# Performance work log

Hardware: AMD Instinct MI355X
Metric: run time of the kernel (lower is better)

## Reference

```python
import jax, jax.numpy as jnp
import numpy as np
from jax import lax


def _gru(x, h, Wi, Wh, bi, bh):
    # PyTorch GRUCell: gates ordered (r, z, n)
    gi = x @ Wi + bi
    gh = h @ Wh + bh
    ir, iz, in_ = jnp.split(gi, 3, axis=-1)
    hr, hz, hn = jnp.split(gh, 3, axis=-1)
    r = jax.nn.sigmoid(ir + hr)
    z = jax.nn.sigmoid(iz + hz)
    n = jnp.tanh(in_ + r * hn)
    return (1.0 - z) * n + z * h


def _mlp(x, W1, b1, W2, b2):
    return jax.nn.leaky_relu(x @ W1 + b1, 0.1) @ W2 + b2


def setup_inputs() -> dict:
    key = jax.random.key(0)
    S, Wn, E, DH, OD = 128, 3968, 128, 512, 2  # scenarios, world agents, embed, dec hidden, out dim
    N, H = S + Wn, 4 * E
    ks = jax.random.split(key, 32)
    rn = lambda k, sh, s: (jax.random.normal(k, sh, jnp.float32) * s)
    # ragged segment ids: every scenario gets >=1 world agent, rest random
    extra = jax.random.randint(ks[0], (Wn - S,), 0, S)
    seg_ids = jnp.sort(jnp.concatenate([jnp.arange(S), extra])).astype(jnp.int32)
    sH = 1.0 / np.sqrt(H)
    return {
        'goals': rn(ks[1], (N, 2), 1.0),
        'agn_dyn': rn(ks[2], (N, E), 1.0),
        'agn_ccls': rn(ks[3], (N, E), 1.0),
        'agn_int': rn(ks[4], (N, E), 1.0),
        'seg_ids': seg_ids,
        'sdc_h0': rn(ks[5], (S, H), 1.0),
        'wld_h0': rn(ks[6], (Wn, H), 1.0),
        'gol_W': rn(ks[7], (2, E), 1.0 / np.sqrt(2.0)),
        'gol_b': rn(ks[8], (E,), 0.01),
        'sdc_Wi': rn(ks[9], (H, 3 * H), sH), 'sdc_Wh': rn(ks[10], (H, 3 * H), sH),
        'sdc_bi': rn(ks[11], (3 * H,), 0.01), 'sdc_bh': rn(ks[12], (3 * H,), 0.01),
        'wld_Wi': rn(ks[13], (H, 3 * H), sH), 'wld_Wh': rn(ks[14], (H, 3 * H), sH),
        'wld_bi': rn(ks[15], (3 * H,), 0.01), 'wld_bh': rn(ks[16], (3 * H,), 0.01),
        'sdc_o1W': rn(ks[17], (H, DH), sH), 'sdc_o1b': rn(ks[18], (DH,), 0.01),
        'sdc_o2W': rn(ks[19], (DH, OD), 1.0 / np.sqrt(DH)), 'sdc_o2b': rn(ks[20], (OD,), 0.01),
        'wld_o1W': rn(ks[21], (H, DH), sH), 'wld_o1b': rn(ks[22], (DH,), 0.01),
        'wld_o2W': rn(ks[23], (DH, OD), 1.0 / np.sqrt(DH)), 'wld_o2b': rn(ks[24], (OD,), 0.01),
    }


def reference(goals, agn_dyn, agn_ccls, agn_int, seg_ids, sdc_h0, wld_h0,
              gol_W, gol_b, sdc_Wi, sdc_Wh, sdc_bi, sdc_bh,
              wld_Wi, wld_Wh, wld_bi, wld_bh,
              sdc_o1W, sdc_o1b, sdc_o2W, sdc_o2b,
              wld_o1W, wld_o1b, wld_o2W, wld_o2b):
    S = sdc_h0.shape[0]
    agn_gol = goals @ gol_W + gol_b                                  # [N, E]
    enc = jnp.concatenate([agn_gol, agn_dyn, agn_ccls, agn_int], 1)  # [N, 4E]
    sdc_h = _gru(enc[:S], sdc_h0, sdc_Wi, sdc_Wh, sdc_bi, sdc_bh)    # step 0
    wld_h = _gru(enc[S:], wld_h0, wld_Wi, wld_Wh, wld_bi, wld_bh)

    def step(carry, _):
        sh, wh = carry
        sdc_in = jax.ops.segment_max(wh, seg_ids, num_segments=S,
                                     indices_are_sorted=True)        # per-scenario max-pool
        wld_in = sh[seg_ids]                                         # broadcast SDC to its group
        sh2 = _gru(sdc_in, sh, sdc_Wi, sdc_Wh, sdc_bi, sdc_bh)
        wh2 = _gru(wld_in, wh, wld_Wi, wld_Wh, wld_bi, wld_bh)
        return (sh2, wh2), (sh2, wh2)

    (_, _), (sdc_hs, wld_hs) = lax.scan(step, (sdc_h, wld_h), None, length=79)
    sdc_all = jnp.concatenate([sdc_h[None], sdc_hs], 0).transpose(1, 0, 2)  # [S, 80, 4E]
    wld_all = jnp.concatenate([wld_h[None], wld_hs], 0).transpose(1, 0, 2)  # [W, 80, 4E]
    out_sdc = _mlp(sdc_all, sdc_o1W, sdc_o1b, sdc_o2W, sdc_o2b)
    out_wld = _mlp(wld_all, wld_o1W, wld_o1b, wld_o2W, wld_o2b)
    return jnp.concatenate([out_sdc, out_wld], 0)                    # [N, 80, out_dim]
```

## Files before the change

kernel.cpp:

```cpp
#include <hip/hip_runtime.h>


typedef __attribute__((ext_vector_type(8))) short short8;
typedef __attribute__((ext_vector_type(4))) float f32x4;
typedef unsigned short u16;
typedef unsigned int u32;

#define DEV __device__ __forceinline__

constexpr int S  = 128;
constexpr int NR = 4096;
constexpr int H  = 512;
constexpr int TH = 1536;
constexpr int SLOT = NR * H;
constexpr int SEGSZ = S * H;

struct P {
  const float *goals, *dyn, *ccls, *inte;
  const int *seg;
  const float *sdc_h0, *wld_h0;
  const float *golW, *golb;
  const float *sdcbi, *sdcbh, *wldbi, *wldbh;
  const float *sdco1b, *sdco2W, *sdco2b;
  const float *wldo1b, *wldo2W, *wldo2b;
  const float *sdcWi, *sdcWh, *wldWi, *wldWh, *sdco1W, *wldo1W;
  float *out;
  float *whf;
  u16   *ring;
  u16   *enc;
  u16   *WT;
  u16   *o1T;
  float *G;
  u32   *segb;
  u16   *segbf;
  float *part;
  int t;
};

DEV u16 f2bf(float f) {
  u32 u = __float_as_uint(f);
  u32 r = u + 0x7FFFu + ((u >> 16) & 1u);
  return (u16)(r >> 16);
}
DEV u32 flipf(float f) {
  u32 u = __float_as_uint(f);
  return (u & 0x80000000u) ? ~u : (u | 0x80000000u);
}
DEV float unflip(u32 s) {
  u32 u = (s & 0x80000000u) ? (s & 0x7FFFFFFFu) : ~s;
  return __uint_as_float(u);
}
DEV float sigm(float x)  { return 1.0f / (1.0f + __expf(-x)); }
DEV float tanh_(float x) { return 2.0f / (1.0f + __expf(-2.0f * x)) - 1.0f; }

DEV f32x4 mfma16(short8 a, short8 b, f32x4 c) {
  return __builtin_amdgcn_mfma_f32_16x16x32_bf16(a, b, c, 0, 0, 0);
}

DEV void gload16(const void* g, void* l) {
  __builtin_amdgcn_global_load_lds(
      (const __attribute__((address_space(1))) void*)g,
      (__attribute__((address_space(3))) void*)l, 16, 0, 0);
}

DEV short8 lds_frag(const u16* lds, int row, int g) {
  return *(const short8*)(lds + row * 64 + ((g ^ (row & 7)) << 3));
}

__global__ __launch_bounds__(256) void k_prep(P p) {
  const int b = blockIdx.x, tid = threadIdx.x;
  __shared__ float ltf[64 * 65];
  if (b < 896) {
    int nt, kt, Nn; const float* src; u16* dst;
    if (b < 768) {
      int m = b / 192, t2 = b % 192;
      nt = t2 % 24; kt = t2 / 24; Nn = TH;
      src = (m == 0) ? p.sdcWi : (m == 1) ? p.sdcWh : (m == 2) ? p.wldWi : p.wldWh;
      dst = p.WT + m * TH * H;
    } else {
      int bb = b - 768, m = bb / 64, t2 = bb % 64;
      nt = t2 % 8; kt = t2 / 8; Nn = H;
      src = m ? p.wldo1W : p.sdco1W;
      dst = p.o1T + m * H * H;
    }
    for (int it = 0; it < 16; ++it) {
      int kl = it * 4 + (tid >> 6), nl = tid & 63;
      ltf[nl * 65 + kl] = src[(kt * 64 + kl) * Nn + nt * 64 + nl];
    }
    __syncthreads();
    for (int it = 0; it < 2; ++it) {
      int nl = it * 32 + (tid >> 3), k8 = (tid & 7) * 8;
      short8 v;
#pragma unroll
      for (int e = 0; e < 8; ++e) v[e] = (short)f2bf(ltf[nl * 65 + k8 + e]);
      *(short8*)(dst + (nt * 64 + nl) * H + kt * 64 + k8) = v;
    }
  } else if (b < 960) {
    int r0 = (b - 896) * 64;
    for (int i = 0; i < 32; ++i) {
      int idx = i * 256 + tid;
      int row = r0 + (idx >> 7), c4 = (idx & 127) * 4;
      float4 v;
      if (c4 < 128) {
        float g0 = p.goals[row * 2], g1 = p.goals[row * 2 + 1];
        v.x = g0 * p.golW[c4]     + g1 * p.golW[128 + c4]     + p.golb[c4];
        v.y = g0 * p.golW[c4 + 1] + g1 * p.golW[128 + c4 + 1] + p.golb[c4 + 1];
        v.z = g0 * p.golW[c4 + 2] + g1 * p.golW[128 + c4 + 2] + p.golb[c4 + 2];
        v.w = g0 * p.golW[c4 + 3] + g1 * p.golW[128 + c4 + 3] + p.golb[c4 + 3];
      } else if (c4 < 256) v = *(const float4*)(p.dyn  + row * 128 + c4 - 128);
      else if (c4 < 384)   v = *(const float4*)(p.ccls + row * 128 + c4 - 256);
      else                 v = *(const float4*)(p.inte + row * 128 + c4 - 384);
      ushort4 o;
      o.x = f2bf(v.x); o.y = f2bf(v.y); o.z = f2bf(v.z); o.w = f2bf(v.w);
      *(ushort4*)(p.enc + row * H + c4) = o;
    }
  } else if (b < 1024) {
    int r0 = (b - 960) * 64;
    for (int i = 0; i < 32; ++i) {
      int idx = i * 256 + tid;
      int row = r0 + (idx >> 7), c4 = (idx & 127) * 4;
      float4 v = (row < S) ? *(const float4*)(p.sdc_h0 + row * H + c4)
                           : *(const float4*)(p.wld_h0 + (row - S) * H + c4);
      *(float4*)(p.whf + SLOT + row * H + c4) = v;
      ushort4 o;
      o.x = f2bf(v.x); o.y = f2bf(v.y); o.z = f2bf(v.z); o.w = f2bf(v.w);
      *(ushort4*)(p.ring + 7 * SLOT + row * H + c4) = o;
    }
  } else {
    int base = (b - 1024) * 16384;
    for (int i = 0; i < 64; ++i) p.segb[base + i * 256 + tid] = 0u;
  }
}

__global__ __launch_bounds__(512) void k_big0(P p) {
  const int b = blockIdx.x, tid = threadIdx.x;
  const int rt = b >> 3, cg = b & 7;
  const bool sdc = rt < 2;
  const int wv = tid >> 6, wm = wv >> 2, wn = wv & 3;
  const int lr = (tid >> 4) & 3, lc = tid & 15;
  __shared__ u16 sm[16384];
  const u16* WiT = p.WT + (sdc ? 0 : 2) * TH * H;
  const u16* WhT = p.WT + (sdc ? 1 : 3) * TH * H;

  f32x4 ai[3][2], ah[3][2];
  f32x4 zero = {0.f, 0.f, 0.f, 0.f};
#pragma unroll
  for (int g = 0; g < 3; ++g)
#pragma unroll
    for (int mt = 0; mt < 2; ++mt) { ai[g][mt] = zero; ah[g][mt] = zero; }

  for (int pass = 0; pass < 2; ++pass) {
    const u16* A  = pass ? (p.ring + 7 * SLOT + rt * 64 * H) : (p.enc + rt * 64 * H);
    const u16* BT = pass ? WhT : WiT;
    for (int kc = 0; kc < H; kc += 64) {
      __syncthreads();
#pragma unroll
      for (int it = 0; it < 4; ++it) {
        int u = it * 512 + tid;
        int gs = (u ^ (u >> 3)) & 7;
        const u16* src;
        if (u < 512) {
          src = A + (u >> 3) * H + kc + gs * 8;
        } else {
          int v = u - 512;
          int g = v >> 9, m = (v >> 3) & 63;
          src = BT + (g * H + cg * 64 + m) * H + kc + gs * 8;
        }
        gload16(src, sm + (it * 512 + (tid & 448)) * 8);
      }
      __syncthreads();
#pragma unroll
      for (int s2 = 0; s2 < 2; ++s2) {
        const int gk = s2 * 4 + lr;
        short8 av[2], bv[3];
#pragma unroll
        for (int mt = 0; mt < 2; ++mt)
          av[mt] = lds_frag(sm, wm * 32 + mt * 16 + lc, gk);
#pragma unroll
        for (int g = 0; g < 3; ++g)
          bv[g] = lds_frag(sm + 4096 + g * 4096, wn * 16 + lc, gk);
#pragma unroll
        for (int g = 0; g < 3; ++g)
#pragma unroll
          for (int mt = 0; mt < 2; ++mt) {
            f32x4 r = pass ? ah[g][mt] : ai[g][mt];
            r = mfma16(av[mt], bv[g], r);
            if (pass) ah[g][mt] = r; else ai[g][mt] = r;
          }
      }
    }
  }
  const float* bi = sdc ? p.sdcbi : p.wldbi;
  const float* bh = sdc ? p.sdcbh : p.wldbh;
  const int col = cg * 64 + wn * 16 + lc;
  const float bir = bi[col], biz = bi[H + col], bin = bi[2 * H + col];
  const float bhr = bh[col], bhz = bh[H + col], bhn = bh[2 * H + col];
#pragma unroll
  for (int mt = 0; mt < 2; ++mt)
#pragma unroll
    for (int i = 0; i < 4; ++i) {
      int grow = rt * 64 + wm * 32 + mt * 16 + lr * 4 + i;
      float r = sigm(ai[0][mt][i] + bir + ah[0][mt][i] + bhr);
      float z = sigm(ai[1][mt][i] + biz + ah[1][mt][i] + bhz);
      float n = tanh_(ai[2][mt][i] + bin + r * (ah[2][mt][i] + bhn));
      float h = p.whf[SLOT + grow * H + col];
      float h2 = (1.f - z) * n + z * h;
      p.whf[grow * H + col] = h2;
      p.ring[grow * H + col] = f2bf(h2);
      if (!sdc) {
        int scen = p.seg[grow - S];
        atomicMax(p.segb + scen * H + col, flipf(h2));
      }
    }
}

__global__ __launch_bounds__(512) void k_small(P p) {
  const int b = blockIdx.x, tid = threadIdx.x;
  if (b >= 48) {
    if ((p.t & 7) != 0 || p.t < 8) return;
    const int base = p.t - 8;
    const int gt2 = (b - 48) * 512 + tid;
    for (int i = gt2; i < 65536; i += 32768) {
      int r = i >> 1, od = i & 1;
      int row = r & 4095, slot = r >> 12;
      float v = p.part[i] + p.part[65536 + i];
      v += (row < S ? p.sdco2b : p.wldo2b)[od];
      p.out[row * 160 + (base + slot) * 2 + od] = v;
    }
    return;
  }
  const int gtid = b * 512 + tid;
  u32* sb = p.segb + (p.t & 1) * SEGSZ;
  if (gtid < 16384) ((uint4*)sb)[gtid] = make_uint4(0u, 0u, 0u, 0u);
  const u32* sp = p.segb + ((p.t - 1) & 1) * SEGSZ;
  if (gtid < 16384) {
    uint4 q = ((const uint4*)sp)[gtid];
    u32 lo = (u32)f2bf(unflip(q.x)) | ((u32)f2bf(unflip(q.y)) << 16);
    u32 hi = (u32)f2bf(unflip(q.z)) | ((u32)f2bf(unflip(q.w)) << 16);
    ((u32*)p.segbf)[gtid * 2]     = lo;
    ((u32*)p.segbf)[gtid * 2 + 1] = hi;
  }
  const int rh = b / 24, nc = b % 24;
  const int wv = tid >> 6, wm = wv >> 2, wn = wv & 3;
  const int lr = (tid >> 4) & 3, lc = tid & 15;
  __shared__ u16 sm[16384];
  const u16* Ab = p.ring + ((p.t - 1) & 7) * SLOT + rh * 64 * H;
  const u16* Wb = p.WT + 2 * TH * H;

  f32x4 acc[2];
  f32x4 zero = {0.f, 0.f, 0.f, 0.f};
  acc[0] = zero; acc[1] = zero;

  for (int kc = 0; kc < H; kc += 128) {
    __syncthreads();
#pragma unroll
    for (int it = 0; it < 4; ++it) {
      int u = it * 512 + tid;
      int q = u >> 9;
      int m = (u >> 3) & 63, g = u & 7;
      int gs = g ^ (m & 7);
      int ko = kc + ((q & 1) << 6) + gs * 8;
      const u16* src = (q < 2) ? (Ab + m * H + ko)
                               : (Wb + (nc * 64 + m) * H + ko);
      gload16(src, sm + (it * 512 + (tid & 448)) * 8);
    }
    __syncthreads();
#pragma unroll
    for (int c = 0; c < 2; ++c)
#pragma unroll
      for (int s2 = 0; s2 < 2; ++s2) {
        const int gk = s2 * 4 + lr;
        short8 bv = lds_frag(sm + (2 + c) * 4096, wn * 16 + lc, gk);
#pragma unroll
        for (int mt = 0; mt < 2; ++mt)
          acc[mt] = mfma16(
              lds_frag(sm + c * 4096, wm * 32 + mt * 16 + lc, gk), bv, acc[mt]);
      }
  }
  const int colb = nc * 64 + wn * 16 + lc;
  const float bi = p.wldbi[colb];
#pragma unroll
  for (int mt = 0; mt < 2; ++mt)
#pragma unroll
    for (int i = 0; i < 4; ++i)
      p.G[(rh * 64 + wm * 32 + mt * 16 + lr * 4 + i) * TH + colb] = acc[mt][i] + bi;
}

__global__ __launch_bounds__(512) void k_big(P p) {
  const int b = blockIdx.x, tid = threadIdx.x;
  const int lr = (tid >> 4) & 3, lc = tid & 15;
  __shared__ u16 sm[16384];
  const int tp = (p.t - 1) & 7, tn = p.t & 7;
  const float* whfP = p.whf + ((p.t - 1) & 1) * SLOT;
  float* whfN = p.whf + (p.t & 1) * SLOT;
  u16* ringN = p.ring + tn * SLOT;

  if (b < 496) {
    const int wv = tid >> 6, wm = wv >> 2, wn = wv & 3;
    const int rt = b >> 3, cg = b & 7;
    const u16* Abase = p.ring + tp * SLOT + (S + rt * 64) * H;
    const u16* Bbase = p.WT + 3 * TH * H;
    f32x4 acc[3][2];
    f32x4 zero = {0.f, 0.f, 0.f, 0.f};
#pragma unroll
    for (int g = 0; g < 3; ++g) { acc[g][0] = zero; acc[g][1] = zero; }

    for (int kc = 0; kc < H; kc += 64) {
      __syncthreads();
#pragma unroll
      for (int it = 0; it < 4; ++it) {
        int u = it * 512 + tid;
        int gs = (u ^ (u >> 3)) & 7;
        const u16* src;
        if (u < 512) {
          src = Abase + (u >> 3) * H + kc + gs * 8;
        } else {
          int v = u - 512;
          int g = v >> 9, m = (v >> 3) & 63;
          src = Bbase + (g * H + cg * 64 + m) * H + kc + gs * 8;
        }
        gload16(src, sm + (it * 512 + (tid & 448)) * 8);
      }
      __syncthreads();
#pragma unroll
      for (int s2 = 0; s2 < 2; ++s2) {
        const int gk = s2 * 4 + lr;
        short8 av[2], bv[3];
#pragma unroll
        for (int mt = 0; mt < 2; ++mt)
          av[mt] = lds_frag(sm, wm * 32 + mt * 16 + lc, gk);
#pragma unroll
        for (int g = 0; g < 3; ++g)
          bv[g] = lds_frag(sm + 4096 + g * 4096, wn * 16 + lc, gk);
#pragma unroll
        for (int g = 0; g < 3; ++g)
#pragma unroll
          for (int mt = 0; mt < 2; ++mt) acc[g][mt] = mfma16(av[mt], bv[g], acc[g][mt]);
      }
    }
    const int col = cg * 64 + wn * 16 + lc;
    const float bhr = p.wldbh[col], bhz = p.wldbh[H + col], bhn = p.wldbh[2 * H + col];
    u32* sb = p.segb + (p.t & 1) * SEGSZ;
    int curSc = -1; float curMx = 0.f;
#pragma unroll
    for (int mt = 0; mt < 2; ++mt)
#pragma unroll
      for (int i = 0; i < 4; ++i) {
        int wrow = rt * 64 + wm * 32 + mt * 16 + lr * 4 + i;
        int grow = S + wrow;
        int scen = p.seg[wrow];
        const float* Gr = p.G + scen * TH;
        float r = sigm(Gr[col]          + acc[0][mt][i] + bhr);
        float z = sigm(Gr[H + col]      + acc[1][mt][i] + bhz);
        float n = tanh_(Gr[2 * H + col] + r * (acc[2][mt][i] + bhn));
        float h = whfP[grow * H + col];
        float h2 = (1.f - z) * n + z * h;
        whfN[grow * H + col] = h2;
        ringN[grow * H + col] = f2bf(h2);
        if (scen == curSc) curMx = fmaxf(curMx, h2);
        else {
          if (curSc >= 0) atomicMax(sb + curSc * H + col, flipf(curMx));
          curSc = scen; curMx = h2;
        }
      }
    atomicMax(sb + curSc * H + col, flipf(curMx));
  } else {
    const int w = tid >> 6;
    if (w >= 4) return;
    const int ab = b - 496, rh = ab >> 5, cgx = ab & 31;
    f32x4 ai[3], ah[3];
    f32x4 zero = {0.f, 0.f, 0.f, 0.f};
#pragma unroll
    for (int g = 0; g < 3; ++g) { ai[g] = zero; ah[g] = zero; }

    for (int pass = 0; pass < 2; ++pass) {
      const u16* A  = pass ? (p.ring + tp * SLOT + rh * 64 * H)
                           : (p.segbf + rh * 64 * H);
      const u16* BT = p.WT + (pass ? 1 : 0) * TH * H;
      for (int kc = 0; kc < H; kc += 64) {
        __syncthreads();
#pragma unroll
        for (int it = 0; it < 4; ++it) {
          int u = it * 256 + tid;
          if (u < 896) {
            int gs = (u ^ (u >> 3)) & 7;
            const u16* src;
            if (u < 512) {
              src = A + (u >> 3) * H + kc + gs * 8;
            } else {
              int v = u - 512;
              int m = v >> 3;
              src = BT + ((m >> 4) * H + cgx * 16 + (m & 15)) * H + kc + gs * 8;
            }
            gload16(src, sm + (it * 256 + (tid & 192)) * 8);
          }
        }
        __syncthreads();
#pragma unroll
        for (int s2 = 0; s2 < 2; ++s2) {
          const int gk = s2 * 4 + lr;
          short8 a = lds_frag(sm, w * 16 + lc, gk);
#pragma unroll
          for (int g = 0; g < 3; ++g) {
            f32x4 r = pass ? ah[g] : ai[g];
            r = mfma16(a, lds_frag(sm + 4096, g * 16 + lc, gk), r);
            if (pass) ah[g] = r; else ai[g] = r;
          }
        }
      }
    }
    const int col = cgx * 16 + lc;
    const float bir = p.sdcbi[col], biz = p.sdcbi[H + col], bin = p.sdcbi[2 * H + col];
    const float bhr = p.sdcbh[col], bhz = p.sdcbh[H + col], bhn = p.sdcbh[2 * H + col];
#pragma unroll
    for (int i = 0; i < 4; ++i) {
      int srow = rh * 64 + w * 16 + lr * 4 + i;
      float r = sigm(ai[0][i] + bir + ah[0][i] + bhr);
      float z = sigm(ai[1][i] + biz + ah[1][i] + bhz);
      float n = tanh_(ai[2][i] + bin + r * (ah[2][i] + bhn));
      float h = whfP[srow * H + col];
      float h2 = (1.f - z) * n + z * h;
      whfN[srow * H + col] = h2;
      ringN[srow * H + col] = f2bf(h2);
    }
  }
}

__global__ __launch_bounds__(512) void k_mlp(P p) {
  const int b = blockIdx.x, tid = threadIdx.x;
  const int rt = b >> 1, ct = b & 1;
  const int slot = rt >> 5, rtile = rt & 31;
  const bool sdc = (rtile == 0);
  const int wv = tid >> 6, wm = wv >> 2, wn = wv & 3;
  const int lr = (tid >> 4) & 3, lc = tid & 15;
  __shared__ u16 sm[24576];
  const u16* A  = p.ring + slot * SLOT + rtile * 128 * H;
  const u16* Bb = p.o1T + (sdc ? 0 : 1) * H * H + (ct * 256) * H;
  const float* o1b = sdc ? p.sdco1b : p.wldo1b;
  const float* o2W = sdc ? p.sdco2W : p.wldo2W;

  f32x4 acc[4][4];
  f32x4 zero = {0.f, 0.f, 0.f, 0.f};
#pragma unroll
  for (int mt = 0; mt < 4; ++mt)
#pragma unroll
    for (int c2 = 0; c2 < 4; ++c2) acc[mt][c2] = zero;

  for (int kc = 0; kc < H; kc += 64) {
    __syncthreads();
#pragma unroll
    for (int it = 0; it < 6; ++it) {
      int u = it * 512 + tid;
      int gs = (u ^ (u >> 3)) & 7;
      const u16* src;
      if (u < 1024) src = A  + (u >> 3) * H + kc + gs * 8;
      else          src = Bb + ((u - 1024) >> 3) * H + kc + gs * 8;
      gload16(src, sm + (it * 512 + (tid & 448)) * 8);
    }
    __syncthreads();
#pragma unroll
    for (int s2 = 0; s2 < 2; ++s2) {
      const int gk = s2 * 4 + lr;
      short8 av[4], bv[4];
#pragma unroll
      for (int mt = 0; mt < 4; ++mt)
        av[mt] = lds_frag(sm, wm * 64 + mt * 16 + lc, gk);
#pragma unroll
      for (int c2 = 0; c2 < 4; ++c2)
        bv[c2] = lds_frag(sm + 8192, wn * 64 + c2 * 16 + lc, gk);
#pragma unroll
      for (int mt = 0; mt < 4; ++mt)
#pragma unroll
        for (int c2 = 0; c2 < 4; ++c2) acc[mt][c2] = mfma16(av[mt], bv[c2], acc[mt][c2]);
    }
  }
  __syncthreads();
  float* red = (float*)sm;
#pragma unroll
  for (int mt = 0; mt < 4; ++mt) {
    float q0[4] = {0.f, 0.f, 0.f, 0.f}, q1[4] = {0.f, 0.f, 0.f, 0.f};
#pragma unroll
    for (int c2 = 0; c2 < 4; ++c2) {
      int col = ct * 256 + wn * 64 + c2 * 16 + lc;
      float b1 = o1b[col], w0 = o2W[col * 2], w1 = o2W[col * 2 + 1];
#pragma unroll
      for (int i = 0; i < 4; ++i) {
        float v = acc[mt][c2][i] + b1;
        v = v > 0.f ? v : 0.1f * v;
        q0[i] += v * w0; q1[i] += v * w1;
      }
    }
#pragma unroll
    for (int off = 1; off < 16; off <<= 1)
#pragma unroll
      for (int i = 0; i < 4; ++i) {
        q0[i] += __shfl_xor(q0[i], off);
        q1[i] += __shfl_xor(q1[i], off);
      }
    if (lc == 0)
#pragma unroll
      for (int i = 0; i < 4; ++i) {
        int row = wm * 64 + mt * 16 + lr * 4 + i;
        red[(wn * 128 + row) * 2 + 0] = q0[i];
        red[(wn * 128 + row) * 2 + 1] = q1[i];
      }
  }
  __syncthreads();
  if (tid < 256) {
    int row = tid >> 1, od = tid & 1;
    float sum = red[(0 * 128 + row) * 2 + od] + red[(1 * 128 + row) * 2 + od] +
                red[(2 * 128 + row) * 2 + od] + red[(3 * 128 + row) * 2 + od];
    int r = slot * 4096 + rtile * 128 + row;
    p.part[ct * 65536 + r * 2 + od] = sum;
  }
}

__global__ __launch_bounds__(256) void k_mlp2(P p) {
  const int gtid = blockIdx.x * 256 + threadIdx.x;
  for (int i = gtid; i < 65536; i += 16384) {
    int r = i >> 1, od = i & 1;
    int row = r & 4095, slot = r >> 12;
    float v = p.part[i] + p.part[65536 + i];
    v += (row < S ? p.sdco2b : p.wldo2b)[od];
    p.out[row * 160 + (p.t + slot) * 2 + od] = v;
  }
}

extern "C" void kernel_launch(void* const* d_in, const int* in_sizes, int n_in,
                              void* d_out, int out_size, void* d_ws, size_t ws_size,
                              hipStream_t stream) {
  P prm;
  prm.goals  = (const float*)d_in[0];
  prm.dyn    = (const float*)d_in[1];
  prm.ccls   = (const float*)d_in[2];
  prm.inte   = (const float*)d_in[3];
  prm.seg    = (const int*)  d_in[4];
  prm.sdc_h0 = (const float*)d_in[5];
  prm.wld_h0 = (const float*)d_in[6];
  prm.golW   = (const float*)d_in[7];
  prm.golb   = (const float*)d_in[8];
  prm.sdcWi  = (const float*)d_in[9];
  prm.sdcWh  = (const float*)d_in[10];
  prm.sdcbi  = (const float*)d_in[11];
  prm.sdcbh  = (const float*)d_in[12];
  prm.wldWi  = (const float*)d_in[13];
  prm.wldWh  = (const float*)d_in[14];
  prm.wldbi  = (const float*)d_in[15];
  prm.wldbh  = (const float*)d_in[16];
  prm.sdco1W = (const float*)d_in[17];
  prm.sdco1b = (const float*)d_in[18];
  prm.sdco2W = (const float*)d_in[19];
  prm.sdco2b = (const float*)d_in[20];
  prm.wldo1W = (const float*)d_in[21];
  prm.wldo1b = (const float*)d_in[22];
  prm.wldo2W = (const float*)d_in[23];
  prm.wldo2b = (const float*)d_in[24];
  prm.out = (float*)d_out;

  char* ws = (char*)d_ws;
  prm.whf   = (float*)(ws + 0);
  prm.ring  = (u16*)  (ws + 16777216);
  prm.enc   = (u16*)  (ws + 50331648);
  prm.WT    = (u16*)  (ws + 54525952);
  prm.o1T   = (u16*)  (ws + 60817408);
  prm.G     = (float*)(ws + 61865984);
  prm.segb  = (u32*)  (ws + 62652416);
  prm.segbf = (u16*)  (ws + 50331648);
  prm.part  = (float*)(ws + 50331648 + 131072);

  prm.t = 0;
  k_prep<<<1028, 256, 0, stream>>>(prm);
  k_big0<<<512, 512, 0, stream>>>(prm);
  for (int t = 1; t < 80; ++t) {
    prm.t = t;
    k_small<<<112, 512, 0, stream>>>(prm);
    k_big<<<560, 512, 0, stream>>>(prm);
    if ((t & 7) == 7) {
      k_mlp<<<512, 512, 0, stream>>>(prm);
    }
  }
  P pm = prm;
  pm.t = 72;
  k_mlp2<<<64, 256, 0, stream>>>(pm);
}
```

Before: 2.254 ms.

## Overlap per-step output MLP with recurrence inside the small-step kernel

Removes the batched k_mlp launch that ran every 8 steps. Instead, each k_small launch gets 128 extra blocks that compute the output MLP for the hidden state from two steps earlier, and 16 blocks that do the final reduction for three steps earlier. A small tail of two kernels finishes the last steps. This hides the MLP work in otherwise idle CUs during the latency-bound recurrence, at the cost of a larger k_small grid and a 4-way column split with an extra partial-sum reduction.

```diff
diff --git a/kernel.cpp b/kernel.cpp
--- a/kernel.cpp
+++ b/kernel.cpp
@@ -67,6 +67,100 @@
   return *(const short8*)(lds + row * 64 + ((g ^ (row & 7)) << 3));
 }
 
+DEV void mlp_partial(const P& p, int st, int rt, int ct, int tid, u16* sm) {
+  const int slot = st & 7, sp = st & 3;
+  const bool sdc = (rt == 0);
+  const int wv = tid >> 6, wm = wv >> 2, wn = wv & 3;
+  const int lr = (tid >> 4) & 3, lc = tid & 15;
+  const u16* A  = p.ring + slot * SLOT + rt * 128 * H;
+  const u16* Bb = p.o1T + (sdc ? 0 : 1) * H * H + (ct * 128) * H;
+  const float* o1b = sdc ? p.sdco1b : p.wldo1b;
+  const float* o2W = sdc ? p.sdco2W : p.wldo2W;
+
+  f32x4 acc[4][2];
+  f32x4 zero = {0.f, 0.f, 0.f, 0.f};
+#pragma unroll
+  for (int mt = 0; mt < 4; ++mt) { acc[mt][0] = zero; acc[mt][1] = zero; }
+
+  for (int kc = 0; kc < H; kc += 64) {
+    __syncthreads();
+#pragma unroll
+    for (int it = 0; it < 4; ++it) {
+      int u = it * 512 + tid;
+      int gs = (u ^ (u >> 3)) & 7;
+      const u16* src;
+      if (u < 1024) src = A  + (u >> 3) * H + kc + gs * 8;
+      else          src = Bb + ((u - 1024) >> 3) * H + kc + gs * 8;
+      gload16(src, sm + (it * 512 + (tid & 448)) * 8);
+    }
+    __syncthreads();
+#pragma unroll
+    for (int s2 = 0; s2 < 2; ++s2) {
+      const int gk = s2 * 4 + lr;
+      short8 av[4], bv[2];
+#pragma unroll
+      for (int mt = 0; mt < 4; ++mt)
+        av[mt] = lds_frag(sm, wm * 64 + mt * 16 + lc, gk);
+#pragma unroll
+      for (int c2 = 0; c2 < 2; ++c2)
+        bv[c2] = lds_frag(sm + 8192, wn * 32 + c2 * 16 + lc, gk);
+#pragma unroll
+      for (int mt = 0; mt < 4; ++mt)
+#pragma unroll
+        for (int c2 = 0; c2 < 2; ++c2) acc[mt][c2] = mfma16(av[mt], bv[c2], acc[mt][c2]);
+    }
+  }
+  __syncthreads();
+  float* red = (float*)sm;
+#pragma unroll
+  for (int mt = 0; mt < 4; ++mt) {
+    float q0[4] = {0.f, 0.f, 0.f, 0.f}, q1[4] = {0.f, 0.f, 0.f, 0.f};
+#pragma unroll
+    for (int c2 = 0; c2 < 2; ++c2) {
+      int col = ct * 128 + wn * 32 + c2 * 16 + lc;
+      float b1 = o1b[col], w0 = o2W[col * 2], w1 = o2W[col * 2 + 1];
+#pragma unroll
+      for (int i = 0; i < 4; ++i) {
+        float v = acc[mt][c2][i] + b1;
+        v = v > 0.f ? v : 0.1f * v;
+        q0[i] += v * w0; q1[i] += v * w1;
+      }
+    }
+#pragma unroll
+    for (int off = 1; off < 16; off <<= 1)
+#pragma unroll
+      for (int i = 0; i < 4; ++i) {
+        q0[i] += __shfl_xor(q0[i], off);
+        q1[i] += __shfl_xor(q1[i], off);
+      }
+    if (lc == 0)
+#pragma unroll
+      for (int i = 0; i < 4; ++i) {
+        int row = wm * 64 + mt * 16 + lr * 4 + i;
+        red[(wn * 128 + row) * 2 + 0] = q0[i];
+        red[(wn * 128 + row) * 2 + 1] = q1[i];
+      }
+  }
+  __syncthreads();
+  if (tid < 256) {
+    int row = tid >> 1, od = tid & 1;
+    float sum = red[(0 * 128 + row) * 2 + od] + red[(1 * 128 + row) * 2 + od] +
+                red[(2 * 128 + row) * 2 + od] + red[(3 * 128 + row) * 2 + od];
+    p.part[sp * 32768 + ct * 8192 + (rt * 128 + row) * 2 + od] = sum;
+  }
+}
+
+DEV void mlp_final(const P& p, int st, int blk, int tid) {
+  const int sp = st & 3;
+  int i = blk * 512 + tid;
+  int row = i >> 1, od = i & 1;
+  const float* pb = p.part + sp * 32768;
+  float v = pb[row * 2 + od] + pb[8192 + row * 2 + od] +
+            pb[16384 + row * 2 + od] + pb[24576 + row * 2 + od];
+  v += (row < S ? p.sdco2b : p.wldo2b)[od];
+  p.out[row * 160 + st * 2 + od] = v;
+}
+
 __global__ __launch_bounds__(256) void k_prep(P p) {
   const int b = blockIdx.x, tid = threadIdx.x;
   __shared__ float ltf[64 * 65];
@@ -216,17 +310,16 @@
 
 __global__ __launch_bounds__(512) void k_small(P p) {
   const int b = blockIdx.x, tid = threadIdx.x;
+  __shared__ u16 sm[16384];
+  if (b >= 64) {
+    if (p.t < 2) return;
+    const int b2 = b - 64;
+    mlp_partial(p, p.t - 2, b2 >> 2, b2 & 3, tid, sm);
+    return;
+  }
   if (b >= 48) {
-    if ((p.t & 7) != 0 || p.t < 8) return;
-    const int base = p.t - 8;
-    const int gt2 = (b - 48) * 512 + tid;
-    for (int i = gt2; i < 65536; i += 32768) {
-      int r = i >> 1, od = i & 1;
-      int row = r & 4095, slot = r >> 12;
-      float v = p.part[i] + p.part[65536 + i];
-      v += (row < S ? p.sdco2b : p.wldo2b)[od];
-      p.out[row * 160 + (base + slot) * 2 + od] = v;
-    }
+    if (p.t < 3) return;
+    mlp_final(p, p.t - 3, b - 48, tid);
     return;
   }
   const int gtid = b * 512 + tid;
@@ -243,7 +336,6 @@
   const int rh = b / 24, nc = b % 24;
   const int wv = tid >> 6, wm = wv >> 2, wn = wv & 3;
   const int lr = (tid >> 4) & 3, lc = tid & 15;
-  __shared__ u16 sm[16384];
   const u16* Ab = p.ring + ((p.t - 1) & 7) * SLOT + rh * 64 * H;
   const u16* Wb = p.WT + 2 * TH * H;
 
@@ -426,104 +518,19 @@
   }
 }
 
-__global__ __launch_bounds__(512) void k_mlp(P p) {
+__global__ __launch_bounds__(512) void k_tailA(P p) {
   const int b = blockIdx.x, tid = threadIdx.x;
-  const int rt = b >> 1, ct = b & 1;
-  const int slot = rt >> 5, rtile = rt & 31;
-  const bool sdc = (rtile == 0);
-  const int wv = tid >> 6, wm = wv >> 2, wn = wv & 3;
-  const int lr = (tid >> 4) & 3, lc = tid & 15;
-  __shared__ u16 sm[24576];
-  const u16* A  = p.ring + slot * SLOT + rtile * 128 * H;
-  const u16* Bb = p.o1T + (sdc ? 0 : 1) * H * H + (ct * 256) * H;
-  const float* o1b = sdc ? p.sdco1b : p.wldo1b;
-  const float* o2W = sdc ? p.sdco2W : p.wldo2W;
-
-  f32x4 acc[4][4];
-  f32x4 zero = {0.f, 0.f, 0.f, 0.f};
-#pragma unroll
-  for (int mt = 0; mt < 4; ++mt)
-#pragma unroll
-    for (int c2 = 0; c2 < 4; ++c2) acc[mt][c2] = zero;
-
-  for (int kc = 0; kc < H; kc += 64) {
-    __syncthreads();
-#pragma unroll
-    for (int it = 0; it < 6; ++it) {
-      int u = it * 512 + tid;
-      int gs = (u ^ (u >> 3)) & 7;
-      const u16* src;
-      if (u < 1024) src = A  + (u >> 3) * H + kc + gs * 8;
-      else          src = Bb + ((u - 1024) >> 3) * H + kc + gs * 8;
-      gload16(src, sm + (it * 512 + (tid & 448)) * 8);
-    }
-    __syncthreads();
-#pragma unroll
-    for (int s2 = 0; s2 < 2; ++s2) {
-      const int gk = s2 * 4 + lr;
-      short8 av[4], bv[4];
-#pragma unroll
-      for (int mt = 0; mt < 4; ++mt)
-        av[mt] = lds_frag(sm, wm * 64 + mt * 16 + lc, gk);
-#pragma unroll
-      for (int c2 = 0; c2 < 4; ++c2)
-        bv[c2] = lds_frag(sm + 8192, wn * 64 + c2 * 16 + lc, gk);
-#pragma unroll
-      for (int mt = 0; mt < 4; ++mt)
-#pragma unroll
-        for (int c2 = 0; c2 < 4; ++c2) acc[mt][c2] = mfma16(av[mt], bv[c2], acc[mt][c2]);
-    }
-  }
-  __syncthreads();
-  float* red = (float*)sm;
-#pragma unroll
-  for (int mt = 0; mt < 4; ++mt) {
-    float q0[4] = {0.f, 0.f, 0.f, 0.f}, q1[4] = {0.f, 0.f, 0.f, 0.f};
-#pragma unroll
-    for (int c2 = 0; c2 < 4; ++c2) {
-      int col = ct * 256 + wn * 64 + c2 * 16 + lc;
-      float b1 = o1b[col], w0 = o2W[col * 2], w1 = o2W[col * 2 + 1];
-#pragma unroll
-      for (int i = 0; i < 4; ++i) {
-        float v = acc[mt][c2][i] + b1;
-        v = v > 0.f ? v : 0.1f * v;
-        q0[i] += v * w0; q1[i] += v * w1;
-      }
-    }
-#pragma unroll
-    for (int off = 1; off < 16; off <<= 1)
-#pragma unroll
-      for (int i = 0; i < 4; ++i) {
-        q0[i] += __shfl_xor(q0[i], off);
-        q1[i] += __shfl_xor(q1[i], off);
-      }
-    if (lc == 0)
-#pragma unroll
-      for (int i = 0; i < 4; ++i) {
-        int row = wm * 64 + mt * 16 + lr * 4 + i;
-        red[(wn * 128 + row) * 2 + 0] = q0[i];
-        red[(wn * 128 + row) * 2 + 1] = q1[i];
-      }
-  }
-  __syncthreads();
-  if (tid < 256) {
-    int row = tid >> 1, od = tid & 1;
-    float sum = red[(0 * 128 + row) * 2 + od] + red[(1 * 128 + row) * 2 + od] +
-                red[(2 * 128 + row) * 2 + od] + red[(3 * 128 + row) * 2 + od];
-    int r = slot * 4096 + rtile * 128 + row;
-    p.part[ct * 65536 + r * 2 + od] = sum;
-  }
-}
-
-__global__ __launch_bounds__(256) void k_mlp2(P p) {
-  const int gtid = blockIdx.x * 256 + threadIdx.x;
-  for (int i = gtid; i < 65536; i += 16384) {
-    int r = i >> 1, od = i & 1;
-    int row = r & 4095, slot = r >> 12;
-    float v = p.part[i] + p.part[65536 + i];
-    v += (row < S ? p.sdco2b : p.wldo2b)[od];
-    p.out[row * 160 + (p.t + slot) * 2 + od] = v;
-  }
+  __shared__ u16 sm[16384];
+  if (b < 256) {
+    int st = 78 + (b >> 7), b2 = b & 127;
+    mlp_partial(p, st, b2 >> 2, b2 & 3, tid, sm);
+  } else {
+    mlp_final(p, 77, b - 256, tid);
+  }
+}
+__global__ __launch_bounds__(512) void k_tailB(P p) {
+  const int b = blockIdx.x, tid = threadIdx.x;
+  mlp_final(p, 78 + (b >> 4), b & 15, tid);
 }
 
 extern "C" void kernel_launch(void* const* d_in, const int* in_sizes, int n_in,
@@ -573,13 +580,9 @@
   k_big0<<<512, 512, 0, stream>>>(prm);
   for (int t = 1; t < 80; ++t) {
     prm.t = t;
-    k_small<<<112, 512, 0, stream>>>(prm);
+    k_small<<<192, 512, 0, stream>>>(prm);
     k_big<<<560, 512, 0, stream>>>(prm);
-    if ((t & 7) == 7) {
-      k_mlp<<<512, 512, 0, stream>>>(prm);
-    }
-  }
-  P pm = prm;
-  pm.t = 72;
-  k_mlp2<<<64, 256, 0, stream>>>(pm);
-}
+  }
+  k_tailA<<<272, 512, 0, stream>>>(prm);
+  k_tailB<<<32, 512, 0, stream>>>(prm);
+}
```

Measured after the change: 2.579 ms. 14.4% more time.
